# Kernel optimization log

Hardware: AMD Instinct MI355X
Metric: run time of the kernel (lower is better)

## Reference

```python
import jax, jax.numpy as jnp
import numpy as np

N = 50000          # nodes
E_RAND = 800000    # random edges (avg degree 16)
D_IN = 128
H = 4              # heads (both layers)
C = 64             # per-head channels (both layers)
NEG_SLOPE = 0.2    # PyG GATConv default leaky_relu slope


def _gat_conv(x, src, dst, W, att_src, att_dst, bias, concat):
    """PyG GATConv (dropout=0, self-loops already in edge list).
    x:[N,Din] W:[Din,H*C] att_*:[H,C] bias:[H*C] or [C]."""
    n = x.shape[0]
    h = (x @ W).reshape(n, H, C)                      # [N,H,C]
    a_src = jnp.sum(h * att_src, axis=-1)             # [N,H]
    a_dst = jnp.sum(h * att_dst, axis=-1)             # [N,H]
    e = jax.nn.leaky_relu(a_src[src] + a_dst[dst], NEG_SLOPE)  # [E,H]
    # segment softmax over incoming edges of each destination node
    m = jax.ops.segment_max(e, dst, num_segments=n)    # [N,H]
    e = jnp.exp(e - m[dst])
    denom = jax.ops.segment_sum(e, dst, num_segments=n)
    alpha = e / (denom[dst] + 1e-16)                   # [E,H]
    msg = h[src] * alpha[..., None]                    # [E,H,C]
    out = jax.ops.segment_sum(msg, dst, num_segments=n)  # [N,H,C]
    if concat:
        out = out.reshape(n, H * C)
    else:
        out = out.mean(axis=1)
    return out + bias


def setup_inputs() -> dict:
    key = jax.random.key(0)
    ks = jax.random.split(key, 10)
    x = jax.random.normal(ks[0], (N, D_IN), jnp.float32)
    src = jax.random.randint(ks[1], (E_RAND,), 0, N)
    dst = jax.random.randint(ks[2], (E_RAND,), 0, N)
    loops = jnp.arange(N)  # add_self_loops=True (PyG default)
    edge_index = jnp.stack([jnp.concatenate([src, loops]),
                            jnp.concatenate([dst, loops])]).astype(jnp.int32)
    g = lambda k, shp, fan: (jax.random.normal(k, shp, jnp.float32) / np.float32(np.sqrt(fan)))
    W1 = g(ks[3], (D_IN, H * C), D_IN)
    att_src1 = g(ks[4], (H, C), C)
    att_dst1 = g(ks[5], (H, C), C)
    b1 = jnp.zeros((H * C,), jnp.float32)
    W2 = g(ks[6], (H * C, H * C), H * C)
    att_src2 = g(ks[7], (H, C), C)
    att_dst2 = g(ks[8], (H, C), C)
    b2 = jnp.zeros((C,), jnp.float32)
    return {"x": x, "edge_index": edge_index,
            "W1": W1, "att_src1": att_src1, "att_dst1": att_dst1, "b1": b1,
            "W2": W2, "att_src2": att_src2, "att_dst2": att_dst2, "b2": b2}


def reference(x, edge_index, W1, att_src1, att_dst1, b1, W2, att_src2, att_dst2, b2):
    src, dst = edge_index[0], edge_index[1]
    h = jax.nn.relu(_gat_conv(x, src, dst, W1, att_src1, att_dst1, b1, concat=True))
    h = jax.nn.relu(_gat_conv(h, src, dst, W2, att_src2, att_dst2, b2, concat=False))
    return jax.nn.softmax(h, axis=1)
```

## Files before the change

kernel.cpp:

```cpp
#include <hip/hip_runtime.h>


typedef __attribute__((ext_vector_type(8))) short short8;
typedef __attribute__((ext_vector_type(4))) float f32x4;
typedef __attribute__((ext_vector_type(2))) float f32x2;

static __device__ __forceinline__ ushort f2bf(float f) {
  uint u = __float_as_uint(f);
  return (ushort)((u + 0x7FFFu + ((u >> 16) & 1u)) >> 16);
}
static __device__ __forceinline__ float bf2f(ushort s) {
  return __uint_as_float(((uint)s) << 16);
}
static __device__ __forceinline__ unsigned char f2fp8(float f) {
  int p = __builtin_amdgcn_cvt_pk_fp8_f32(f, f, 0, false);
  return (unsigned char)(p & 0xFF);
}
static __device__ __forceinline__ uint4 cvt8bf(const float4& a, const float4& b) {
  uint4 hh;
  hh.x = (uint)f2bf(a.x) | ((uint)f2bf(a.y) << 16);
  hh.y = (uint)f2bf(a.z) | ((uint)f2bf(a.w) << 16);
  hh.z = (uint)f2bf(b.x) | ((uint)f2bf(b.y) << 16);
  hh.w = (uint)f2bf(b.z) | ((uint)f2bf(b.w) << 16);
  return hh;
}

__global__ __launch_bounds__(256)
void k_prep_hist(const float* __restrict__ W1, const float* __restrict__ W2,
                 ushort* __restrict__ w1th, ushort* __restrict__ w1tl,
                 ushort* __restrict__ w2th, ushort* __restrict__ w2tl,
                 const int* __restrict__ dstv, int* __restrict__ cnt,
                 int* __restrict__ pe, int E) {
  const int b = blockIdx.x;
  if (b < 128) {
    int gid = b * 256 + threadIdx.x;
    int c = gid & 255, k = gid >> 8;
    float w = W1[(size_t)k * 256 + c];
    ushort h = f2bf(w);
    w1th[(size_t)c * 128 + k] = h;
    w1tl[(size_t)c * 128 + k] = f2bf(w - bf2f(h));
  } else if (b < 384) {
    int gid = (b - 128) * 256 + threadIdx.x;
    int c = gid & 255, k = gid >> 8;
    float w = W2[(size_t)k * 256 + c];
    ushort h = f2bf(w);
    w2th[(size_t)c * 256 + k] = h;
    w2tl[(size_t)c * 256 + k] = f2bf(w - bf2f(h));
  } else {
    int i = (b - 384) * 256 + threadIdx.x;
    if (i < E) pe[i] = atomicAdd(&cnt[dstv[i]], 1);
  }
}

__global__ __launch_bounds__(256)
void k_scan(const int* __restrict__ cnt, int* __restrict__ rowptr,
            int* __restrict__ bsum, int* __restrict__ bflag, int N, int E) {
  __shared__ int sm[256];
  __shared__ int s_prev;
  const int b = blockIdx.x, tid = threadIdx.x;
  const int gid = b * 256 + tid;
  int v = (gid < N) ? cnt[gid] : 0;
  sm[tid] = v;
  __syncthreads();
  for (int off = 1; off < 256; off <<= 1) {
    int t = (tid >= off) ? sm[tid - off] : 0;
    __syncthreads();
    sm[tid] += t;
    __syncthreads();
  }
  if (tid == 255) {
    atomicExch(&bsum[b], sm[255]);
    __threadfence();
    atomicExch(&bflag[b], 1);
  }
  if (tid == 0) s_prev = 0;
  __syncthreads();
  if (tid < b) {
    while (atomicAdd(&bflag[tid], 0) == 0) {}
    atomicAdd(&s_prev, atomicAdd(&bsum[tid], 0));
  }
  __syncthreads();
  if (gid < N) rowptr[gid] = s_prev + sm[tid] - v;
  if (gid == 0) rowptr[N] = E;
}

template <int FP32A>
static __device__ __forceinline__
void gemm_body(int bid, const void* __restrict__ Aany,
               const ushort* __restrict__ Bth, const ushort* __restrict__ Btl,
               unsigned char* __restrict__ hout, int Nrows, int K,
               const float* __restrict__ att_s, const float* __restrict__ att_d,
               float* __restrict__ a_s, float* __restrict__ a_d) {
  __shared__ ushort As_h[128][40];

  const int nrb = (Nrows + 127) >> 7;
  const int rb = (bid >> 4) * 8 + (bid & 7);
  const int ch = (bid >> 3) & 1;
  if (rb >= nrb) return;
  const int row0 = rb * 128;
  const int col0 = ch * 128;

  const int t = threadIdx.x;
  const int lane = t & 63;
  const int w = t >> 6;
  const int wr = (w >> 1) * 64;
  const int wc = (w & 1) * 64;
  const int lrow = t >> 2;
  const int kc = (t & 3) * 8;

  const float*  Af = (const float*)Aany;
  const ushort* Ah = (const ushort*)Aany;

  f32x4 acc[4][4] = {};

  float4 pf[2][2];
  uint4 pa_h[2];
  const uint4 z4 = make_uint4(0, 0, 0, 0);
#pragma unroll
  for (int p = 0; p < 2; p++) {
    int gr = row0 + p * 64 + lrow;
    if (FP32A) {
      if (gr < Nrows) {
        const float* ap = Af + (size_t)gr * K + kc;
        pf[p][0] = *(const float4*)(ap);
        pf[p][1] = *(const float4*)(ap + 4);
      } else {
        pf[p][0] = make_float4(0.f, 0.f, 0.f, 0.f);
        pf[p][1] = pf[p][0];
      }
    } else {
      if (gr < Nrows) pa_h[p] = *(const uint4*)(Ah + (size_t)gr * K + kc);
      else pa_h[p] = z4;
    }
  }

  const int fr = lane & 15;
  const int fq = lane >> 4;
  const ushort* bb_h = Bth + (size_t)(col0 + wc + fr) * K + fq * 8;
  const ushort* bb_l = Btl + (size_t)(col0 + wc + fr) * K + fq * 8;

  for (int k0 = 0; k0 < K; k0 += 32) {
#pragma unroll
    for (int p = 0; p < 2; p++) {
      uint4 hh;
      if (FP32A) hh = cvt8bf(pf[p][0], pf[p][1]);
      else hh = pa_h[p];
      *(uint4*)(&As_h[p * 64 + lrow][kc]) = hh;
    }
    __syncthreads();

    if (k0 + 32 < K) {
#pragma unroll
      for (int p = 0; p < 2; p++) {
        int gr = row0 + p * 64 + lrow;
        if (FP32A) {
          if (gr < Nrows) {
            const float* ap = Af + (size_t)gr * K + k0 + 32 + kc;
            pf[p][0] = *(const float4*)(ap);
            pf[p][1] = *(const float4*)(ap + 4);
          } else {
            pf[p][0] = make_float4(0.f, 0.f, 0.f, 0.f);
            pf[p][1] = pf[p][0];
          }
        } else {
          if (gr < Nrows)
            pa_h[p] = *(const uint4*)(Ah + (size_t)gr * K + k0 + 32 + kc);
          else pa_h[p] = z4;
        }
      }
    }

    short8 fb_h[4], fb_l[4];
#pragma unroll
    for (int c = 0; c < 4; c++) {
      fb_h[c] = *(const short8*)(bb_h + (size_t)c * 16 * K + k0);
      fb_l[c] = *(const short8*)(bb_l + (size_t)c * 16 * K + k0);
    }
    short8 fa_h[4];
#pragma unroll
    for (int r = 0; r < 4; r++)
      fa_h[r] = *(const short8*)(&As_h[wr + r * 16 + fr][fq * 8]);
#pragma unroll
    for (int r = 0; r < 4; r++)
#pragma unroll
      for (int c = 0; c < 4; c++) {
        acc[r][c] = __builtin_amdgcn_mfma_f32_16x16x32_bf16(fa_h[r], fb_h[c], acc[r][c], 0, 0, 0);
        acc[r][c] = __builtin_amdgcn_mfma_f32_16x16x32_bf16(fa_h[r], fb_l[c], acc[r][c], 0, 0, 0);
      }
    __syncthreads();
  }

#pragma unroll
  for (int r = 0; r < 4; r++)
#pragma unroll
    for (int c = 0; c < 4; c++) {
      int colg = col0 + wc + c * 16 + fr;
#pragma unroll
      for (int reg = 0; reg < 4; reg++) {
        int gr = row0 + wr + r * 16 + fq * 4 + reg;
        if (gr < Nrows)
          hout[(size_t)gr * 256 + colg] = f2fp8(acc[r][c][reg]);
      }
    }

  const int head = (col0 + wc) >> 6;
  float asv[4], adv[4];
#pragma unroll
  for (int c = 0; c < 4; c++) {
    asv[c] = att_s[col0 + wc + c * 16 + fr];
    adv[c] = att_d[col0 + wc + c * 16 + fr];
  }
#pragma unroll
  for (int r = 0; r < 4; r++)
#pragma unroll
    for (int reg = 0; reg < 4; reg++) {
      float ps = 0.f, pd = 0.f;
#pragma unroll
      for (int c = 0; c < 4; c++) {
        ps += acc[r][c][reg] * asv[c];
        pd += acc[r][c][reg] * adv[c];
      }
      ps += __shfl_xor(ps, 1); pd += __shfl_xor(pd, 1);
      ps += __shfl_xor(ps, 2); pd += __shfl_xor(pd, 2);
      ps += __shfl_xor(ps, 4); pd += __shfl_xor(pd, 4);
      ps += __shfl_xor(ps, 8); pd += __shfl_xor(pd, 8);
      if (fr == 0) {
        int gr = row0 + wr + r * 16 + fq * 4 + reg;
        if (gr < Nrows) {
          a_s[(size_t)gr * 4 + head] = ps;
          a_d[(size_t)gr * 4 + head] = pd;
        }
      }
    }
}

__global__ __launch_bounds__(256)
void k_gemm1_scatter(const float* __restrict__ x,
                     const ushort* __restrict__ Bth,
                     const ushort* __restrict__ Btl,
                     unsigned char* __restrict__ hout, int Nrows,
                     const float* __restrict__ att_s,
                     const float* __restrict__ att_d,
                     float* __restrict__ a_s, float* __restrict__ a_d,
                     const int* __restrict__ srcv, const int* __restrict__ dstv,
                     const int* __restrict__ rowptr, const int* __restrict__ pe,
                     int* __restrict__ col, int E, int gemm_blocks) {
  if ((int)blockIdx.x < gemm_blocks) {
    gemm_body<1>(blockIdx.x, x, Bth, Btl, hout, Nrows, 128,
                 att_s, att_d, a_s, a_d);
  } else {
    int base = ((int)blockIdx.x - gemm_blocks) * 1024 + threadIdx.x;
#pragma unroll
    for (int k = 0; k < 4; k++) {
      int i = base + k * 256;
      if (i < E) col[rowptr[dstv[i]] + pe[i]] = srcv[i];
    }
  }
}

__global__ __launch_bounds__(256)
void k_gemm2(const ushort* __restrict__ Ah,
             const ushort* __restrict__ Bth, const ushort* __restrict__ Btl,
             unsigned char* __restrict__ hout, int Nrows,
             const float* __restrict__ att_s, const float* __restrict__ att_d,
             float* __restrict__ a_s, float* __restrict__ a_d) {
  gemm_body<0>(blockIdx.x, Ah, Bth, Btl, hout, Nrows, 256,
               att_s, att_d, a_s, a_d);
}

template <int LAYER>
__global__ __launch_bounds__(256)
void k_aggr(const unsigned char* __restrict__ hsrc,
            const int* __restrict__ rowptr, const int* __restrict__ col,
            const float* __restrict__ a_s, const float* __restrict__ a_d,
            const float* __restrict__ bias,
            ushort* __restrict__ out_h, float* __restrict__ outp, int N) {
  __shared__ int   s_sh[4][64];
  __shared__ float w_sh[4][256];
  const int wv = threadIdx.x >> 6;
  const int lane = threadIdx.x & 63;
  const int node = blockIdx.x * 4 + wv;
  if (node >= N) return;
  const int hd = lane >> 4;
  const int beg = rowptr[node], end = rowptr[node + 1];
  const float4 adst = *(const float4*)(a_d + (size_t)node * 4);

  float4 acc = make_float4(0.f, 0.f, 0.f, 0.f);
  float wsum = 0.f;
  const char* hbase = (const char*)hsrc + lane * 4;

  for (int c0 = beg; c0 < end; c0 += 64) {
    int nc = min(64, end - c0);
    int s = 0;
    float4 w4 = make_float4(0.f, 0.f, 0.f, 0.f);
    if (lane < nc) {
      s = col[c0 + lane];
      float4 a = *(const float4*)(a_s + (size_t)s * 4);
      float e0 = a.x + adst.x; e0 = e0 > 0.f ? e0 : 0.2f * e0;
      float e1 = a.y + adst.y; e1 = e1 > 0.f ? e1 : 0.2f * e1;
      float e2 = a.z + adst.z; e2 = e2 > 0.f ? e2 : 0.2f * e2;
      float e3 = a.w + adst.w; e3 = e3 > 0.f ? e3 : 0.2f * e3;
      w4 = make_float4(__expf(e0), __expf(e1), __expf(e2), __expf(e3));
    }
    s_sh[wv][lane] = s;
    *(float4*)(&w_sh[wv][lane * 4]) = w4;
    asm volatile("s_waitcnt lgkmcnt(0)" ::: "memory");

    const float* wrow = &w_sh[wv][hd];
    const int*   srow = &s_sh[wv][0];
    int j = 0;
    for (; j + 4 <= nc; j += 4) {
      int sj0 = srow[j], sj1 = srow[j + 1], sj2 = srow[j + 2], sj3 = srow[j + 3];
      float w0 = wrow[4 * j],      w1 = wrow[4 * j + 4];
      float w2 = wrow[4 * j + 8],  w3 = wrow[4 * j + 12];
      uint p0 = *(const uint*)(hbase + ((size_t)((uint)sj0 << 8)));
      uint p1 = *(const uint*)(hbase + ((size_t)((uint)sj1 << 8)));
      uint p2 = *(const uint*)(hbase + ((size_t)((uint)sj2 << 8)));
      uint p3 = *(const uint*)(hbase + ((size_t)((uint)sj3 << 8)));
      f32x2 l0 = __builtin_amdgcn_cvt_pk_f32_fp8(p0, false);
      f32x2 h0 = __builtin_amdgcn_cvt_pk_f32_fp8(p0, true);
      f32x2 l1 = __builtin_amdgcn_cvt_pk_f32_fp8(p1, false);
      f32x2 h1 = __builtin_amdgcn_cvt_pk_f32_fp8(p1, true);
      f32x2 l2 = __builtin_amdgcn_cvt_pk_f32_fp8(p2, false);
      f32x2 h2 = __builtin_amdgcn_cvt_pk_f32_fp8(p2, true);
      f32x2 l3 = __builtin_amdgcn_cvt_pk_f32_fp8(p3, false);
      f32x2 h3 = __builtin_amdgcn_cvt_pk_f32_fp8(p3, true);
      wsum += w0 + w1 + w2 + w3;
      acc.x += w0 * l0.x; acc.y += w0 * l0.y; acc.z += w0 * h0.x; acc.w += w0 * h0.y;
      acc.x += w1 * l1.x; acc.y += w1 * l1.y; acc.z += w1 * h1.x; acc.w += w1 * h1.y;
      acc.x += w2 * l2.x; acc.y += w2 * l2.y; acc.z += w2 * h2.x; acc.w += w2 * h2.y;
      acc.x += w3 * l3.x; acc.y += w3 * l3.y; acc.z += w3 * h3.x; acc.w += w3 * h3.y;
    }
    for (; j < nc; j++) {
      int sj = srow[j];
      float ww = wrow[4 * j];
      uint p = *(const uint*)(hbase + ((size_t)((uint)sj << 8)));
      f32x2 lo = __builtin_amdgcn_cvt_pk_f32_fp8(p, false);
      f32x2 hi = __builtin_amdgcn_cvt_pk_f32_fp8(p, true);
      wsum += ww;
      acc.x += ww * lo.x; acc.y += ww * lo.y;
      acc.z += ww * hi.x; acc.w += ww * hi.y;
    }
  }

  float inv = 1.0f / wsum;
  float4 v = make_float4(acc.x * inv, acc.y * inv, acc.z * inv, acc.w * inv);

  if (LAYER == 1) {
    const float4 bv = *(const float4*)(bias + lane * 4);
    v.x = fmaxf(v.x + bv.x, 0.f);
    v.y = fmaxf(v.y + bv.y, 0.f);
    v.z = fmaxf(v.z + bv.z, 0.f);
    v.w = fmaxf(v.w + bv.w, 0.f);
    ushort4 h;
    h.x = f2bf(v.x); h.y = f2bf(v.y); h.z = f2bf(v.z); h.w = f2bf(v.w);
    *(ushort4*)(out_h + (size_t)node * 256 + lane * 4) = h;
  } else {
    v.x += __shfl_xor(v.x, 16); v.y += __shfl_xor(v.y, 16);
    v.z += __shfl_xor(v.z, 16); v.w += __shfl_xor(v.w, 16);
    v.x += __shfl_xor(v.x, 32); v.y += __shfl_xor(v.y, 32);
    v.z += __shfl_xor(v.z, 32); v.w += __shfl_xor(v.w, 32);
    const int c4 = (lane & 15) * 4;
    const float4 bv = *(const float4*)(bias + c4);
    v.x = fmaxf(v.x * 0.25f + bv.x, 0.f);
    v.y = fmaxf(v.y * 0.25f + bv.y, 0.f);
    v.z = fmaxf(v.z * 0.25f + bv.z, 0.f);
    v.w = fmaxf(v.w * 0.25f + bv.w, 0.f);
    float mx = fmaxf(fmaxf(v.x, v.y), fmaxf(v.z, v.w));
    for (int off = 8; off >= 1; off >>= 1) mx = fmaxf(mx, __shfl_xor(mx, off));
    v.x = __expf(v.x - mx); v.y = __expf(v.y - mx);
    v.z = __expf(v.z - mx); v.w = __expf(v.w - mx);
    float sum = v.x + v.y + v.z + v.w;
    for (int off = 8; off >= 1; off >>= 1) sum += __shfl_xor(sum, off);
    float is = 1.0f / sum;
    v.x *= is; v.y *= is; v.z *= is; v.w *= is;
    if (lane < 16) *(float4*)(outp + (size_t)node * 64 + c4) = v;
  }
}


extern "C" void kernel_launch(void* const* d_in, const int* in_sizes, int n_in,
                              void* d_out, int out_size, void* d_ws, size_t ws_size,
                              hipStream_t stream) {
  const float* x   = (const float*)d_in[0];
  const int*   ei  = (const int*)d_in[1];
  const float* W1  = (const float*)d_in[2];
  const float* as1 = (const float*)d_in[3];
  const float* ad1 = (const float*)d_in[4];
  const float* b1  = (const float*)d_in[5];
  const float* W2  = (const float*)d_in[6];
  const float* as2 = (const float*)d_in[7];
  const float* ad2 = (const float*)d_in[8];
  const float* b2  = (const float*)d_in[9];
  float* out = (float*)d_out;

  const int N = in_sizes[0] / 128;
  const int E = in_sizes[1] / 2;
  const int* srcv = ei;
  const int* dstv = ei + E;

  unsigned char* h8 = (unsigned char*)d_ws;
  ushort* hb   = (ushort*)(h8 + (size_t)N * 256);
  ushort* w1th = hb + (size_t)N * 256;
  ushort* w1tl = w1th + 256 * 128;
  ushort* w2th = w1tl + 256 * 128;
  ushort* w2tl = w2th + 256 * 256;
  float*  zbuf = (float*)(w2tl + 256 * 256);
  float* a_s1 = zbuf;
  float* a_d1 = a_s1 + (size_t)N * 4;
  float* a_s2 = a_d1 + (size_t)N * 4;
  float* a_d2 = a_s2 + (size_t)N * 4;
  int* rowptr = (int*)(zbuf + (size_t)N * 16);
  int* cnt    = rowptr + (N + 4);
  int* bflag  = cnt + N;
  int* bsum   = bflag + 256;
  int* pe     = bsum + 256;
  int* colx   = pe + E;

  const int nb = (N + 255) / 256;
  const int eb = (E + 255) / 256;
  const int eb4 = (E + 1023) / 1024;

  const int nrb = (N + 127) / 128;
  const int gemm_blocks = ((nrb + 7) / 8) * 16;
  const int wb = (N + 3) / 4;

  hipMemsetAsync(cnt, 0, ((size_t)N + 256) * 4, stream);
  k_prep_hist<<<384 + eb, 256, 0, stream>>>(W1, W2, w1th, w1tl, w2th, w2tl,
                                            dstv, cnt, pe, E);
  k_scan<<<nb, 256, 0, stream>>>(cnt, rowptr, bsum, bflag, N, E);
  k_gemm1_scatter<<<gemm_blocks + eb4, 256, 0, stream>>>(
      x, w1th, w1tl, h8, N, as1, ad1, a_s1, a_d1,
      srcv, dstv, rowptr, pe, colx, E, gemm_blocks);
  k_aggr<1><<<wb, 256, 0, stream>>>(h8, rowptr, colx, a_s1, a_d1, b1,
                                    hb, nullptr, N);
  k_gemm2<<<gemm_blocks, 256, 0, stream>>>(hb, w2th, w2tl, h8, N,
                                           as2, ad2, a_s2, a_d2);
  k_aggr<2><<<wb, 256, 0, stream>>>(h8, rowptr, colx, a_s2, a_d2, b2,
                                    nullptr, out, N);
}
```

Baseline: 298.4 us.

## Split GEMM tile across 8 waves and double-buffer LDS A tile

The shared GEMM body now runs with 512 threads per block. Each of the 8 waves computes a 32x64 sub-tile instead of 64x64, which halves the accumulator registers per wave and adds more waves to hide latency. The LDS A buffer is double-buffered, so each k-step needs one barrier instead of two, and each thread now stages a single row chunk. The edge-scatter branch of the fused launch is resized to 2048 edges per block to match the larger block. In exchange, each wave reloads the same B fragments, so B traffic from global/L2 goes up.

```diff
diff --git a/kernel.cpp b/kernel.cpp
--- a/kernel.cpp
+++ b/kernel.cpp
@@ -91,7 +91,7 @@
                unsigned char* __restrict__ hout, int Nrows, int K,
                const float* __restrict__ att_s, const float* __restrict__ att_d,
                float* __restrict__ a_s, float* __restrict__ a_d) {
-  __shared__ ushort As_h[128][40];
+  __shared__ ushort As_h[2][128][40];
 
   const int nrb = (Nrows + 127) >> 7;
   const int rb = (bid >> 4) * 8 + (bid & 7);
@@ -103,7 +103,7 @@
   const int t = threadIdx.x;
   const int lane = t & 63;
   const int w = t >> 6;
-  const int wr = (w >> 1) * 64;
+  const int wr = (w >> 1) * 32;
   const int wc = (w & 1) * 64;
   const int lrow = t >> 2;
   const int kc = (t & 3) * 8;
@@ -111,27 +111,21 @@
   const float*  Af = (const float*)Aany;
   const ushort* Ah = (const ushort*)Aany;
 
-  f32x4 acc[4][4] = {};
-
-  float4 pf[2][2];
-  uint4 pa_h[2];
-  const uint4 z4 = make_uint4(0, 0, 0, 0);
-#pragma unroll
-  for (int p = 0; p < 2; p++) {
-    int gr = row0 + p * 64 + lrow;
-    if (FP32A) {
-      if (gr < Nrows) {
-        const float* ap = Af + (size_t)gr * K + kc;
-        pf[p][0] = *(const float4*)(ap);
-        pf[p][1] = *(const float4*)(ap + 4);
-      } else {
-        pf[p][0] = make_float4(0.f, 0.f, 0.f, 0.f);
-        pf[p][1] = pf[p][0];
-      }
-    } else {
-      if (gr < Nrows) pa_h[p] = *(const uint4*)(Ah + (size_t)gr * K + kc);
-      else pa_h[p] = z4;
-    }
+  f32x4 acc[2][4] = {};
+
+  const int gr_s = row0 + lrow;
+  const bool arow_ok = (gr_s < Nrows);
+
+  float4 pf0 = make_float4(0.f, 0.f, 0.f, 0.f), pf1 = pf0;
+  uint4 pa = make_uint4(0, 0, 0, 0);
+  if (FP32A) {
+    if (arow_ok) {
+      const float* ap = Af + (size_t)gr_s * K + kc;
+      pf0 = *(const float4*)(ap);
+      pf1 = *(const float4*)(ap + 4);
+    }
+  } else {
+    if (arow_ok) pa = *(const uint4*)(Ah + (size_t)gr_s * K + kc);
   }
 
   const int fr = lane & 15;
@@ -139,34 +133,23 @@
   const ushort* bb_h = Bth + (size_t)(col0 + wc + fr) * K + fq * 8;
   const ushort* bb_l = Btl + (size_t)(col0 + wc + fr) * K + fq * 8;
 
+  int buf = 0;
   for (int k0 = 0; k0 < K; k0 += 32) {
-#pragma unroll
-    for (int p = 0; p < 2; p++) {
-      uint4 hh;
-      if (FP32A) hh = cvt8bf(pf[p][0], pf[p][1]);
-      else hh = pa_h[p];
-      *(uint4*)(&As_h[p * 64 + lrow][kc]) = hh;
-    }
+    uint4 hh;
+    if (FP32A) hh = cvt8bf(pf0, pf1);
+    else hh = pa;
+    *(uint4*)(&As_h[buf][lrow][kc]) = hh;
     __syncthreads();
 
     if (k0 + 32 < K) {
-#pragma unroll
-      for (int p = 0; p < 2; p++) {
-        int gr = row0 + p * 64 + lrow;
-        if (FP32A) {
-          if (gr < Nrows) {
-            const float* ap = Af + (size_t)gr * K + k0 + 32 + kc;
-            pf[p][0] = *(const float4*)(ap);
-            pf[p][1] = *(const float4*)(ap + 4);
-          } else {
-            pf[p][0] = make_float4(0.f, 0.f, 0.f, 0.f);
-            pf[p][1] = pf[p][0];
-          }
-        } else {
-          if (gr < Nrows)
-            pa_h[p] = *(const uint4*)(Ah + (size_t)gr * K + k0 + 32 + kc);
-          else pa_h[p] = z4;
+      if (FP32A) {
+        if (arow_ok) {
+          const float* ap = Af + (size_t)gr_s * K + k0 + 32 + kc;
+          pf0 = *(const float4*)(ap);
+          pf1 = *(const float4*)(ap + 4);
         }
+      } else {
+        if (arow_ok) pa = *(const uint4*)(Ah + (size_t)gr_s * K + k0 + 32 + kc);
       }
     }
 
@@ -176,22 +159,22 @@
       fb_h[c] = *(const short8*)(bb_h + (size_t)c * 16 * K + k0);
       fb_l[c] = *(const short8*)(bb_l + (size_t)c * 16 * K + k0);
     }
-    short8 fa_h[4];
-#pragma unroll
-    for (int r = 0; r < 4; r++)
-      fa_h[r] = *(const short8*)(&As_h[wr + r * 16 + fr][fq * 8]);
-#pragma unroll
-    for (int r = 0; r < 4; r++)
+    short8 fa_h[2];
+#pragma unroll
+    for (int r = 0; r < 2; r++)
+      fa_h[r] = *(const short8*)(&As_h[buf][wr + r * 16 + fr][fq * 8]);
+#pragma unroll
+    for (int r = 0; r < 2; r++)
 #pragma unroll
       for (int c = 0; c < 4; c++) {
         acc[r][c] = __builtin_amdgcn_mfma_f32_16x16x32_bf16(fa_h[r], fb_h[c], acc[r][c], 0, 0, 0);
         acc[r][c] = __builtin_amdgcn_mfma_f32_16x16x32_bf16(fa_h[r], fb_l[c], acc[r][c], 0, 0, 0);
       }
-    __syncthreads();
-  }
-
-#pragma unroll
-  for (int r = 0; r < 4; r++)
+    buf ^= 1;
+  }
+
+#pragma unroll
+  for (int r = 0; r < 2; r++)
 #pragma unroll
     for (int c = 0; c < 4; c++) {
       int colg = col0 + wc + c * 16 + fr;
@@ -211,7 +194,7 @@
     adv[c] = att_d[col0 + wc + c * 16 + fr];
   }
 #pragma unroll
-  for (int r = 0; r < 4; r++)
+  for (int r = 0; r < 2; r++)
 #pragma unroll
     for (int reg = 0; reg < 4; reg++) {
       float ps = 0.f, pd = 0.f;
@@ -234,7 +217,7 @@
     }
 }
 
-__global__ __launch_bounds__(256)
+__global__ __launch_bounds__(512)
 void k_gemm1_scatter(const float* __restrict__ x,
                      const ushort* __restrict__ Bth,
                      const ushort* __restrict__ Btl,
@@ -249,16 +232,16 @@
     gemm_body<1>(blockIdx.x, x, Bth, Btl, hout, Nrows, 128,
                  att_s, att_d, a_s, a_d);
   } else {
-    int base = ((int)blockIdx.x - gemm_blocks) * 1024 + threadIdx.x;
+    int base = ((int)blockIdx.x - gemm_blocks) * 2048 + threadIdx.x;
 #pragma unroll
     for (int k = 0; k < 4; k++) {
-      int i = base + k * 256;
+      int i = base + k * 512;
       if (i < E) col[rowptr[dstv[i]] + pe[i]] = srcv[i];
     }
   }
 }
 
-__global__ __launch_bounds__(256)
+__global__ __launch_bounds__(512)
 void k_gemm2(const ushort* __restrict__ Ah,
              const ushort* __restrict__ Bth, const ushort* __restrict__ Btl,
              unsigned char* __restrict__ hout, int Nrows,
@@ -419,7 +402,7 @@
 
   const int nb = (N + 255) / 256;
   const int eb = (E + 255) / 256;
-  const int eb4 = (E + 1023) / 1024;
+  const int eb4 = (E + 2047) / 2048;
 
   const int nrb = (N + 127) / 128;
   const int gemm_blocks = ((nrb + 7) / 8) * 16;
@@ -429,12 +412,12 @@
   k_prep_hist<<<384 + eb, 256, 0, stream>>>(W1, W2, w1th, w1tl, w2th, w2tl,
                                             dstv, cnt, pe, E);
   k_scan<<<nb, 256, 0, stream>>>(cnt, rowptr, bsum, bflag, N, E);
-  k_gemm1_scatter<<<gemm_blocks + eb4, 256, 0, stream>>>(
+  k_gemm1_scatter<<<gemm_blocks + eb4, 512, 0, stream>>>(
       x, w1th, w1tl, h8, N, as1, ad1, a_s1, a_d1,
       srcv, dstv, rowptr, pe, colx, E, gemm_blocks);
   k_aggr<1><<<wb, 256, 0, stream>>>(h8, rowptr, colx, a_s1, a_d1, b1,
                                     hb, nullptr, N);
-  k_gemm2<<<gemm_blocks, 256, 0, stream>>>(hb, w2th, w2tl, h8, N,
+  k_gemm2<<<gemm_blocks, 512, 0, stream>>>(hb, w2th, w2tl, h8, N,
                                            as2, ad2, a_s2, a_d2);
   k_aggr<2><<<wb, 256, 0, stream>>>(h8, rowptr, colx, a_s2, a_d2, b2,
                                     nullptr, out, N);
```

Result: slower. 321.0 us (+7.6%).

## Pre-convert x to bf16 and load GEMM A fragments directly from global memory

Applied to the files above, without the earlier changes.

The fp32-to-bf16 conversion of x moves into the prep/histogram kernel as extra blocks, writing a bf16 copy of x into the workspace. The GEMM body then drops the LDS staging buffer and its barriers, loads A fragments straight from global memory per wave, and fully unrolls the K loop with K as a template parameter. Launch bounds now request two blocks per CU. The aim is to remove the LDS round trip and syncs, at the cost of an extra pass over x, redundant global A reads across the two column-waves, and possible register pressure.

```diff
diff --git a/kernel.cpp b/kernel.cpp
--- a/kernel.cpp
+++ b/kernel.cpp
@@ -30,8 +30,11 @@
                  ushort* __restrict__ w1th, ushort* __restrict__ w1tl,
                  ushort* __restrict__ w2th, ushort* __restrict__ w2tl,
                  const int* __restrict__ dstv, int* __restrict__ cnt,
-                 int* __restrict__ pe, int E) {
+                 int* __restrict__ pe, int E,
+                 const float* __restrict__ x, ushort* __restrict__ xb,
+                 int ng ) {
   const int b = blockIdx.x;
+  const int eb = (E + 255) >> 8;
   if (b < 128) {
     int gid = b * 256 + threadIdx.x;
     int c = gid & 255, k = gid >> 8;
@@ -46,9 +49,16 @@
     ushort h = f2bf(w);
     w2th[(size_t)c * 256 + k] = h;
     w2tl[(size_t)c * 256 + k] = f2bf(w - bf2f(h));
-  } else {
+  } else if (b < 384 + eb) {
     int i = (b - 384) * 256 + threadIdx.x;
     if (i < E) pe[i] = atomicAdd(&cnt[dstv[i]], 1);
+  } else {
+    int i = (b - 384 - eb) * 256 + threadIdx.x;
+    if (i < ng) {
+      const float4* xp = (const float4*)x + (size_t)i * 2;
+      float4 a = xp[0], bb = xp[1];
+      ((uint4*)xb)[i] = cvt8bf(a, bb);
+    }
   }
 }
 
@@ -84,15 +94,13 @@
   if (gid == 0) rowptr[N] = E;
 }
 
-template <int FP32A>
+template <int K>
 static __device__ __forceinline__
-void gemm_body(int bid, const void* __restrict__ Aany,
+void gemm_body(int bid, const ushort* __restrict__ Ah,
                const ushort* __restrict__ Bth, const ushort* __restrict__ Btl,
-               unsigned char* __restrict__ hout, int Nrows, int K,
+               unsigned char* __restrict__ hout, int Nrows,
                const float* __restrict__ att_s, const float* __restrict__ att_d,
                float* __restrict__ a_s, float* __restrict__ a_d) {
-  __shared__ ushort As_h[128][40];
-
   const int nrb = (Nrows + 127) >> 7;
   const int rb = (bid >> 4) * 8 + (bid & 7);
   const int ch = (bid >> 3) & 1;
@@ -105,89 +113,40 @@
   const int w = t >> 6;
   const int wr = (w >> 1) * 64;
   const int wc = (w & 1) * 64;
-  const int lrow = t >> 2;
-  const int kc = (t & 3) * 8;
-
-  const float*  Af = (const float*)Aany;
-  const ushort* Ah = (const ushort*)Aany;
-
-  f32x4 acc[4][4] = {};
-
-  float4 pf[2][2];
-  uint4 pa_h[2];
-  const uint4 z4 = make_uint4(0, 0, 0, 0);
-#pragma unroll
-  for (int p = 0; p < 2; p++) {
-    int gr = row0 + p * 64 + lrow;
-    if (FP32A) {
-      if (gr < Nrows) {
-        const float* ap = Af + (size_t)gr * K + kc;
-        pf[p][0] = *(const float4*)(ap);
-        pf[p][1] = *(const float4*)(ap + 4);
-      } else {
-        pf[p][0] = make_float4(0.f, 0.f, 0.f, 0.f);
-        pf[p][1] = pf[p][0];
-      }
-    } else {
-      if (gr < Nrows) pa_h[p] = *(const uint4*)(Ah + (size_t)gr * K + kc);
-      else pa_h[p] = z4;
-    }
-  }
 
   const int fr = lane & 15;
   const int fq = lane >> 4;
+
+  const ushort* arow[4];
+#pragma unroll
+  for (int r = 0; r < 4; r++) {
+    int gr = row0 + wr + r * 16 + fr;
+    gr = gr < Nrows ? gr : Nrows - 1;
+    arow[r] = Ah + (size_t)gr * K + fq * 8;
+  }
   const ushort* bb_h = Bth + (size_t)(col0 + wc + fr) * K + fq * 8;
   const ushort* bb_l = Btl + (size_t)(col0 + wc + fr) * K + fq * 8;
 
+  f32x4 acc[4][4] = {};
+
+#pragma unroll
   for (int k0 = 0; k0 < K; k0 += 32) {
-#pragma unroll
-    for (int p = 0; p < 2; p++) {
-      uint4 hh;
-      if (FP32A) hh = cvt8bf(pf[p][0], pf[p][1]);
-      else hh = pa_h[p];
-      *(uint4*)(&As_h[p * 64 + lrow][kc]) = hh;
-    }
-    __syncthreads();
-
-    if (k0 + 32 < K) {
-#pragma unroll
-      for (int p = 0; p < 2; p++) {
-        int gr = row0 + p * 64 + lrow;
-        if (FP32A) {
-          if (gr < Nrows) {
-            const float* ap = Af + (size_t)gr * K + k0 + 32 + kc;
-            pf[p][0] = *(const float4*)(ap);
-            pf[p][1] = *(const float4*)(ap + 4);
-          } else {
-            pf[p][0] = make_float4(0.f, 0.f, 0.f, 0.f);
-            pf[p][1] = pf[p][0];
-          }
-        } else {
-          if (gr < Nrows)
-            pa_h[p] = *(const uint4*)(Ah + (size_t)gr * K + k0 + 32 + kc);
-          else pa_h[p] = z4;
-        }
+    short8 fa[4], fbh[4], fbl[4];
+#pragma unroll
+    for (int r = 0; r < 4; r++)
+      fa[r] = *(const short8*)(arow[r] + k0);
+#pragma unroll
+    for (int c = 0; c < 4; c++) {
+      fbh[c] = *(const short8*)(bb_h + (size_t)c * 16 * K + k0);
+      fbl[c] = *(const short8*)(bb_l + (size_t)c * 16 * K + k0);
+    }
+#pragma unroll
+    for (int r = 0; r < 4; r++)
+#pragma unroll
+      for (int c = 0; c < 4; c++) {
+        acc[r][c] = __builtin_amdgcn_mfma_f32_16x16x32_bf16(fa[r], fbh[c], acc[r][c], 0, 0, 0);
+        acc[r][c] = __builtin_amdgcn_mfma_f32_16x16x32_bf16(fa[r], fbl[c], acc[r][c], 0, 0, 0);
       }
-    }
-
-    short8 fb_h[4], fb_l[4];
-#pragma unroll
-    for (int c = 0; c < 4; c++) {
-      fb_h[c] = *(const short8*)(bb_h + (size_t)c * 16 * K + k0);
-      fb_l[c] = *(const short8*)(bb_l + (size_t)c * 16 * K + k0);
-    }
-    short8 fa_h[4];
-#pragma unroll
-    for (int r = 0; r < 4; r++)
-      fa_h[r] = *(const short8*)(&As_h[wr + r * 16 + fr][fq * 8]);
-#pragma unroll
-    for (int r = 0; r < 4; r++)
-#pragma unroll
-      for (int c = 0; c < 4; c++) {
-        acc[r][c] = __builtin_amdgcn_mfma_f32_16x16x32_bf16(fa_h[r], fb_h[c], acc[r][c], 0, 0, 0);
-        acc[r][c] = __builtin_amdgcn_mfma_f32_16x16x32_bf16(fa_h[r], fb_l[c], acc[r][c], 0, 0, 0);
-      }
-    __syncthreads();
   }
 
 #pragma unroll
@@ -234,8 +193,8 @@
     }
 }
 
-__global__ __launch_bounds__(256)
-void k_gemm1_scatter(const float* __restrict__ x,
+__global__ __launch_bounds__(256, 2)
+void k_gemm1_scatter(const ushort* __restrict__ xb,
                      const ushort* __restrict__ Bth,
                      const ushort* __restrict__ Btl,
                      unsigned char* __restrict__ hout, int Nrows,
@@ -246,8 +205,8 @@
                      const int* __restrict__ rowptr, const int* __restrict__ pe,
                      int* __restrict__ col, int E, int gemm_blocks) {
   if ((int)blockIdx.x < gemm_blocks) {
-    gemm_body<1>(blockIdx.x, x, Bth, Btl, hout, Nrows, 128,
-                 att_s, att_d, a_s, a_d);
+    gemm_body<128>(blockIdx.x, xb, Bth, Btl, hout, Nrows,
+                   att_s, att_d, a_s, a_d);
   } else {
     int base = ((int)blockIdx.x - gemm_blocks) * 1024 + threadIdx.x;
 #pragma unroll
@@ -258,14 +217,14 @@
   }
 }
 
-__global__ __launch_bounds__(256)
+__global__ __launch_bounds__(256, 2)
 void k_gemm2(const ushort* __restrict__ Ah,
              const ushort* __restrict__ Bth, const ushort* __restrict__ Btl,
              unsigned char* __restrict__ hout, int Nrows,
              const float* __restrict__ att_s, const float* __restrict__ att_d,
              float* __restrict__ a_s, float* __restrict__ a_d) {
-  gemm_body<0>(blockIdx.x, Ah, Bth, Btl, hout, Nrows, 256,
-               att_s, att_d, a_s, a_d);
+  gemm_body<256>(blockIdx.x, Ah, Bth, Btl, hout, Nrows,
+                 att_s, att_d, a_s, a_d);
 }
 
 template <int LAYER>
@@ -416,21 +375,24 @@
   int* bsum   = bflag + 256;
   int* pe     = bsum + 256;
   int* colx   = pe + E;
+  ushort* xb  = (ushort*)(colx + E);
 
   const int nb = (N + 255) / 256;
   const int eb = (E + 255) / 256;
   const int eb4 = (E + 1023) / 1024;
+  const int ng = N * 16;
+  const int xcb = (ng + 255) / 256;
 
   const int nrb = (N + 127) / 128;
   const int gemm_blocks = ((nrb + 7) / 8) * 16;
   const int wb = (N + 3) / 4;
 
   hipMemsetAsync(cnt, 0, ((size_t)N + 256) * 4, stream);
-  k_prep_hist<<<384 + eb, 256, 0, stream>>>(W1, W2, w1th, w1tl, w2th, w2tl,
-                                            dstv, cnt, pe, E);
+  k_prep_hist<<<384 + eb + xcb, 256, 0, stream>>>(
+      W1, W2, w1th, w1tl, w2th, w2tl, dstv, cnt, pe, E, x, xb, ng);
   k_scan<<<nb, 256, 0, stream>>>(cnt, rowptr, bsum, bflag, N, E);
   k_gemm1_scatter<<<gemm_blocks + eb4, 256, 0, stream>>>(
-      x, w1th, w1tl, h8, N, as1, ad1, a_s1, a_d1,
+      xb, w1th, w1tl, h8, N, as1, ad1, a_s1, a_d1,
       srcv, dstv, rowptr, pe, colx, E, gemm_blocks);
   k_aggr<1><<<wb, 256, 0, stream>>>(h8, rowptr, colx, a_s1, a_d1, b1,
                                     hb, nullptr, N);
```

Result: slower. 308.3 us (+3.3%).
